# Optimization experiments

Measured on AMD Instinct MI355X. Metric: run time of the kernel, lower is better.

The kernel has to match this reference:

```python
import jax, jax.numpy as jnp
import numpy as np

START_AGE = 0
END_AGE = 100
LAMBDA_1 = 0.2
LAMBDA_2 = 0.05
EPS = 1e-3

N = 524288
WIDTH = END_AGE + 1 - START_AGE  # 101


def setup_inputs() -> dict:
    key = jax.random.key(0)
    k1, k2 = jax.random.split(key)
    inp = jax.random.normal(k1, (N, WIDTH), dtype=jnp.float32)
    target = jax.random.randint(k2, (N,), 0, WIDTH, dtype=jnp.int32)
    return {"input": inp, "target": target}


def reference(input, target):
    # softmax over age bins
    p = jax.nn.softmax(input, axis=1)                                  # [N, W]
    a = jnp.arange(START_AGE, END_AGE + 1, dtype=jnp.float32)          # [W]
    tf = target.astype(jnp.float32)
    # expected age per sample
    mean = jnp.sum(p * a, axis=1)                                      # [N]
    mean_loss = jnp.mean((mean - tf) ** 2) / 2.0
    # vectorized one-hot gather: prob of ground-truth bin
    prob_gt = jnp.take_along_axis(p, target[:, None].astype(jnp.int32), axis=1)  # [N,1]
    # mask of bins with prob strictly below the GT prob; detached in the original
    mask = jax.lax.stop_gradient((p < prob_gt).astype(p.dtype))        # [N, W]
    p_not_K = mask * p
    residue_loss = jnp.mean(jnp.sum(-(p_not_K + EPS) * jnp.log(p_not_K + EPS), axis=1))
    batch_average_K = jnp.sum(mask == 0).astype(jnp.float32) / N
    return (LAMBDA_1 * mean_loss, LAMBDA_2 * residue_loss, batch_average_K)
```

## Files before the change

kernel.cpp:

```cpp
#include <hip/hip_runtime.h>

#define N_ROWS   524288
#define W_BINS   101
#define EPS_F    1e-3f
#define RPB      64
#define NBLK     (N_ROWS / RPB)
#define TILE_F   (RPB * W_BINS)

typedef const float __attribute__((address_space(1)))* gptr_t;
typedef float __attribute__((address_space(3)))* sptr_t;

__global__ __launch_bounds__(64) void mrl_main(const float* __restrict__ x,
                                               const int* __restrict__ tgt,
                                               float4* __restrict__ partial) {
    __shared__ float sm[TILE_F];
    const int lane = threadIdx.x;
    const float* gbase = x + (size_t)blockIdx.x * TILE_F;

    #pragma unroll
    for (int q = 0; q < 25; ++q) {
        __builtin_amdgcn_global_load_lds((gptr_t)(gbase + q * 256 + lane * 4),
                                         (sptr_t)(sm + q * 256), 16, 0, 0);
    }
    if (lane < 16) {
        __builtin_amdgcn_global_load_lds((gptr_t)(gbase + 6400 + lane * 4),
                                         (sptr_t)(sm + 6400), 16, 0, 0);
    }

    const int row = blockIdx.x * RPB + lane;
    const int t   = tgt[row];

    __syncthreads();

    const float* r = sm + lane * W_BINS;

    float se0 = 0.f, se1 = 0.f, sa0 = 0.f, sa1 = 0.f;
    #pragma unroll
    for (int i = 0; i < 100; i += 2) {
        float e0 = __expf(r[i]);
        float e1 = __expf(r[i + 1]);
        se0 += e0; sa0 += e0 * (float)i;
        se1 += e1; sa1 += e1 * (float)(i + 1);
    }
    {
        float e = __expf(r[100]);
        se0 += e; sa0 += e * 100.0f;
    }
    const float se  = se0 + se1;
    const float sea = sa0 + sa1;

    const float egt = __expf(r[t]);
    const float inv = __builtin_amdgcn_rcpf(se);
    const float d   = sea * inv - (float)t;
    float sq = d * d;

    float rc0 = 0.f, rc1 = 0.f;
    int   k   = 0;
    #pragma unroll
    for (int i = 0; i < 100; i += 2) {
        float e0 = __expf(r[i]);
        float e1 = __expf(r[i + 1]);
        bool  l0 = e0 < egt, l1 = e1 < egt;
        float q0 = (l0 ? e0 * inv : 0.f) + EPS_F;
        float q1 = (l1 ? e1 * inv : 0.f) + EPS_F;
        rc0 -= q0 * __logf(q0);
        rc1 -= q1 * __logf(q1);
        k   += (l0 ? 0 : 1) + (l1 ? 0 : 1);
    }
    {
        float e = __expf(r[100]);
        bool  l = e < egt;
        float q = (l ? e * inv : 0.f) + EPS_F;
        rc0 -= q * __logf(q);
        k   += l ? 0 : 1;
    }
    float rc = rc0 + rc1;
    float kf = (float)k;

    #pragma unroll
    for (int off = 32; off >= 1; off >>= 1) {
        sq += __shfl_xor(sq, off);
        rc += __shfl_xor(rc, off);
        kf += __shfl_xor(kf, off);
    }
    if (lane == 0) {
        partial[blockIdx.x] = make_float4(sq, rc, kf, 0.0f);
    }
}

__global__ __launch_bounds__(256) void mrl_reduce(const float4* __restrict__ partial,
                                                  float* __restrict__ out) {
    double s = 0.0, r = 0.0, k = 0.0;
    for (int i = threadIdx.x; i < NBLK; i += 256) {
        float4 v = partial[i];
        s += (double)v.x; r += (double)v.y; k += (double)v.z;
    }
    #pragma unroll
    for (int off = 32; off >= 1; off >>= 1) {
        s += __shfl_xor(s, off);
        r += __shfl_xor(r, off);
        k += __shfl_xor(k, off);
    }
    __shared__ double sd[12];
    const int w = threadIdx.x >> 6;
    if ((threadIdx.x & 63) == 0) { sd[w * 3 + 0] = s; sd[w * 3 + 1] = r; sd[w * 3 + 2] = k; }
    __syncthreads();
    if (threadIdx.x == 0) {
        double S = sd[0] + sd[3] + sd[6] + sd[9];
        double R = sd[1] + sd[4] + sd[7] + sd[10];
        double K = sd[2] + sd[5] + sd[8] + sd[11];
        const double n = (double)N_ROWS;
        out[0] = (float)(0.1  * (S / n));
        out[1] = (float)(0.05 * (R / n));
        out[2] = (float)(K / n);
    }
}

extern "C" void kernel_launch(void* const* d_in, const int* in_sizes, int n_in,
                              void* d_out, int out_size, void* d_ws, size_t ws_size,
                              hipStream_t stream) {
    const float* x   = (const float*)d_in[0];
    const int*   tgt = (const int*)d_in[1];
    float*  out     = (float*)d_out;
    float4* partial = (float4*)d_ws;

    mrl_main<<<NBLK, RPB, 0, stream>>>(x, tgt, partial);
    mrl_reduce<<<1, 256, 0, stream>>>(partial, out);
}
```

Measured before the change: 303.1 us.

## Split each row across two half-waves and cache exponentials in registers

Each row is now handled by two threads, each covering about half the 101 bins, with 128 threads per block. Partial sums and the ground-truth exp are combined with a cross-half shuffle. The second pass reuses exponentials kept in a 50-entry register array instead of recomputing exp, and the reduce kernel uses 1024 threads. The intent is to halve per-thread serial work and remove the redundant exp calls, at the cost of higher register pressure, an extra block-level sync and a shared-memory combine.

Measured after the change: 294.7 us. 1.03x faster.

```diff
diff --git a/kernel.cpp b/kernel.cpp
--- a/kernel.cpp
+++ b/kernel.cpp
@@ -6,71 +6,87 @@
 #define RPB      64
 #define NBLK     (N_ROWS / RPB)
 #define TILE_F   (RPB * W_BINS)
+#define THREADS  128
 
 typedef const float __attribute__((address_space(1)))* gptr_t;
 typedef float __attribute__((address_space(3)))* sptr_t;
 
-__global__ __launch_bounds__(64) void mrl_main(const float* __restrict__ x,
-                                               const int* __restrict__ tgt,
-                                               float4* __restrict__ partial) {
-    __shared__ float sm[TILE_F];
-    const int lane = threadIdx.x;
+__global__ __launch_bounds__(THREADS) void mrl_main(const float* __restrict__ x,
+                                                    const int* __restrict__ tgt,
+                                                    float4* __restrict__ partial) {
+    __shared__ float  sm[TILE_F];
+    __shared__ float4 wsum[2];
+    const int tid = threadIdx.x;
+    const int wv  = tid >> 6;
     const float* gbase = x + (size_t)blockIdx.x * TILE_F;
 
     #pragma unroll
-    for (int q = 0; q < 25; ++q) {
-        __builtin_amdgcn_global_load_lds((gptr_t)(gbase + q * 256 + lane * 4),
-                                         (sptr_t)(sm + q * 256), 16, 0, 0);
+    for (int q = 0; q < 12; ++q) {
+        __builtin_amdgcn_global_load_lds((gptr_t)(gbase + q * 512 + tid * 4),
+                                         (sptr_t)(sm + q * 512 + (wv << 8)), 16, 0, 0);
     }
-    if (lane < 16) {
-        __builtin_amdgcn_global_load_lds((gptr_t)(gbase + 6400 + lane * 4),
-                                         (sptr_t)(sm + 6400), 16, 0, 0);
+    if (tid < 80) {
+        __builtin_amdgcn_global_load_lds((gptr_t)(gbase + 6144 + tid * 4),
+                                         (sptr_t)(sm + 6144 + (wv << 8)), 16, 0, 0);
     }
 
-    const int row = blockIdx.x * RPB + lane;
-    const int t   = tgt[row];
+    const int r = (wv << 5) | (tid & 31);
+    const int h = (tid >> 5) & 1;
+    const int t = tgt[blockIdx.x * RPB + r];
 
     __syncthreads();
 
-    const float* r = sm + lane * W_BINS;
+    const float* rp = sm + r * W_BINS + h * 51;
+    const int    cb = h * 51;
 
-    float se0 = 0.f, se1 = 0.f, sa0 = 0.f, sa1 = 0.f;
+    float e[50];
+    float e50 = 0.f;
+    float se0 = 0.f, se1 = 0.f, sa0 = 0.f, sa1 = 0.f, eg = 0.f;
     #pragma unroll
-    for (int i = 0; i < 100; i += 2) {
-        float e0 = __expf(r[i]);
-        float e1 = __expf(r[i + 1]);
-        se0 += e0; sa0 += e0 * (float)i;
-        se1 += e1; sa1 += e1 * (float)(i + 1);
+    for (int i = 0; i < 50; i += 2) {
+        float v0 = rp[i], v1 = rp[i + 1];
+        float E0 = __expf(v0);
+        float E1 = __expf(v1);
+        e[i] = E0; e[i + 1] = E1;
+        se0 += E0; sa0 += E0 * (float)(cb + i);
+        se1 += E1; sa1 += E1 * (float)(cb + i + 1);
+        eg = (cb + i     == t) ? E0 : eg;
+        eg = (cb + i + 1 == t) ? E1 : eg;
     }
-    {
-        float e = __expf(r[100]);
-        se0 += e; sa0 += e * 100.0f;
+    if (h == 0) {
+        e50 = __expf(rp[50]);
+        se0 += e50; sa0 += e50 * 50.0f;
+        eg = (t == 50) ? e50 : eg;
     }
-    const float se  = se0 + se1;
-    const float sea = sa0 + sa1;
+    float se  = se0 + se1;
+    float sea = sa0 + sa1;
 
-    const float egt = __expf(r[t]);
+    se  += __shfl_xor(se, 32);
+    sea += __shfl_xor(sea, 32);
+    const float egt = eg + __shfl_xor(eg, 32);
     const float inv = __builtin_amdgcn_rcpf(se);
-    const float d   = sea * inv - (float)t;
-    float sq = d * d;
+
+    float sq = 0.f;
+    if (h == 0) {
+        float d = sea * inv - (float)t;
+        sq = d * d;
+    }
 
     float rc0 = 0.f, rc1 = 0.f;
     int   k   = 0;
     #pragma unroll
-    for (int i = 0; i < 100; i += 2) {
-        float e0 = __expf(r[i]);
-        float e1 = __expf(r[i + 1]);
-        bool  l0 = e0 < egt, l1 = e1 < egt;
-        float q0 = (l0 ? e0 * inv : 0.f) + EPS_F;
-        float q1 = (l1 ? e1 * inv : 0.f) + EPS_F;
+    for (int i = 0; i < 50; i += 2) {
+        float E0 = e[i], E1 = e[i + 1];
+        bool  l0 = E0 < egt, l1 = E1 < egt;
+        float q0 = (l0 ? E0 * inv : 0.f) + EPS_F;
+        float q1 = (l1 ? E1 * inv : 0.f) + EPS_F;
         rc0 -= q0 * __logf(q0);
         rc1 -= q1 * __logf(q1);
         k   += (l0 ? 0 : 1) + (l1 ? 0 : 1);
     }
-    {
-        float e = __expf(r[100]);
-        bool  l = e < egt;
-        float q = (l ? e * inv : 0.f) + EPS_F;
+    if (h == 0) {
+        bool  l = e50 < egt;
+        float q = (l ? e50 * inv : 0.f) + EPS_F;
         rc0 -= q * __logf(q);
         k   += l ? 0 : 1;
     }
@@ -83,16 +99,20 @@
         rc += __shfl_xor(rc, off);
         kf += __shfl_xor(kf, off);
     }
-    if (lane == 0) {
-        partial[blockIdx.x] = make_float4(sq, rc, kf, 0.0f);
+    if ((tid & 63) == 0) wsum[wv] = make_float4(sq, rc, kf, 0.f);
+    __syncthreads();
+    if (tid == 0) {
+        float4 a = wsum[0], b = wsum[1];
+        partial[blockIdx.x] = make_float4(a.x + b.x, a.y + b.y, a.z + b.z, 0.f);
     }
 }
 
-__global__ __launch_bounds__(256) void mrl_reduce(const float4* __restrict__ partial,
-                                                  float* __restrict__ out) {
+__global__ __launch_bounds__(1024) void mrl_reduce(const float4* __restrict__ partial,
+                                                   float* __restrict__ out) {
     double s = 0.0, r = 0.0, k = 0.0;
-    for (int i = threadIdx.x; i < NBLK; i += 256) {
-        float4 v = partial[i];
+    #pragma unroll
+    for (int i = 0; i < 8; ++i) {
+        float4 v = partial[threadIdx.x + (i << 10)];
         s += (double)v.x; r += (double)v.y; k += (double)v.z;
     }
     #pragma unroll
@@ -101,14 +121,14 @@
         r += __shfl_xor(r, off);
         k += __shfl_xor(k, off);
     }
-    __shared__ double sd[12];
+    __shared__ double sd[48];
     const int w = threadIdx.x >> 6;
     if ((threadIdx.x & 63) == 0) { sd[w * 3 + 0] = s; sd[w * 3 + 1] = r; sd[w * 3 + 2] = k; }
     __syncthreads();
     if (threadIdx.x == 0) {
-        double S = sd[0] + sd[3] + sd[6] + sd[9];
-        double R = sd[1] + sd[4] + sd[7] + sd[10];
-        double K = sd[2] + sd[5] + sd[8] + sd[11];
+        double S = 0.0, R = 0.0, K = 0.0;
+        #pragma unroll
+        for (int i = 0; i < 16; ++i) { S += sd[i * 3]; R += sd[i * 3 + 1]; K += sd[i * 3 + 2]; }
         const double n = (double)N_ROWS;
         out[0] = (float)(0.1  * (S / n));
         out[1] = (float)(0.05 * (R / n));
@@ -124,6 +144,6 @@
     float*  out     = (float*)d_out;
     float4* partial = (float4*)d_ws;
 
-    mrl_main<<<NBLK, RPB, 0, stream>>>(x, tgt, partial);
-    mrl_reduce<<<1, 256, 0, stream>>>(partial, out);
+    mrl_main<<<NBLK, THREADS, 0, stream>>>(x, tgt, partial);
+    mrl_reduce<<<1, 1024, 0, stream>>>(partial, out);
 }
```
